# Performance work log

Hardware: AMD Instinct MI355X
Metric: run time of the kernel (lower is better)

The kernel has to match this reference:

```python
import jax, jax.numpy as jnp
import numpy as np

N = 100000   # nodes
E = 1600000  # edges (avg in-degree 16)
IN, H, C = 128, 128, 40
K = 2        # TAGConv hops (DGL default)


def setup_inputs() -> dict:
    key = jax.random.key(0)
    ks = jax.random.split(key, 7)
    in_feat = jax.random.normal(ks[0], (N, IN), dtype=jnp.float32)
    src = jax.random.randint(ks[1], (E,), 0, N)
    dst = jax.random.randint(ks[2], (E,), 0, N)
    # TAGConv linear: concat of (K+1) hop features -> out
    W1 = jax.random.normal(ks[3], ((K + 1) * IN, H), dtype=jnp.float32) / np.float32(np.sqrt((K + 1) * IN))
    b1 = jnp.zeros((H,), dtype=jnp.float32)
    W2 = jax.random.normal(ks[4], ((K + 1) * H, C), dtype=jnp.float32) / np.float32(np.sqrt((K + 1) * H))
    b2 = jnp.zeros((C,), dtype=jnp.float32)
    return {"in_feat": in_feat, "src": src, "dst": dst,
            "W1": W1, "b1": b1, "W2": W2, "b2": b2}


def _tagconv(x, src, dst, norm, W, b):
    feats = [x]
    h = x
    for _ in range(K):
        h = norm[:, None] * h                               # [N, d]
        h = jax.ops.segment_sum(h[src], dst, num_segments=N)  # SpMM via gather+scatter
        h = norm[:, None] * h
        feats.append(h)
    return jnp.concatenate(feats, axis=-1) @ W + b


def reference(in_feat, src, dst, W1, b1, W2, b2):
    deg = jax.ops.segment_sum(jnp.ones((E,), jnp.float32), dst, num_segments=N)
    norm = jnp.where(deg > 0, deg ** -0.5, 0.0)             # D^{-1/2}, inf -> 0
    h = jax.nn.relu(_tagconv(in_feat, src, dst, norm, W1, b1))
    h = jax.nn.relu(_tagconv(h, src, dst, norm, W2, b2))
    return jnp.mean(h, axis=0, keepdims=True)               # dgl.mean_nodes -> [1, C]
```

## Files before the change

kernel.cpp:

```cpp
#include <hip/hip_runtime.h>

typedef unsigned short u16;
typedef __attribute__((ext_vector_type(8))) short bf16x8;
typedef __attribute__((ext_vector_type(4))) float f32x4;

#define CSR_CHUNK 12288

__device__ inline u16 f2bf(float f) {
    union { float f; unsigned u; } v; v.f = f;
    unsigned r = v.u + 0x7fff + ((v.u >> 16) & 1);
    return (u16)(r >> 16);
}
__device__ inline float bflo(unsigned u) {
    union { unsigned u; float f; } v; v.u = u << 16; return v.f;
}
__device__ inline float bfhi(unsigned u) {
    union { unsigned u; float f; } v; v.u = u & 0xffff0000u; return v.f;
}
__device__ inline float bfs(u16 x) { return bflo((unsigned)x); }
__device__ inline unsigned pk(float lo, float hi) {
    return (unsigned)f2bf(lo) | ((unsigned)f2bf(hi) << 16);
}

__global__ __launch_bounds__(256) void prep_k(
    const float* __restrict__ X, u16* __restrict__ Xb, long n4,
    const float* __restrict__ W1, u16* __restrict__ Wp1,
    const float* __restrict__ W2, u16* __restrict__ Wp2,
    int* __restrict__ bcnt, int nzero) {
    int b = blockIdx.x;
    int t = threadIdx.x;
    if (b < 4) {
        int i = b * 256 + t;
        if (i < nzero) bcnt[i] = 0;
        return;
    }
    b -= 4;
    if (b < 192) {
        int i = b * 256 + t;
        int m = i >> 14, r = i & 16383;
        int jj = r & 7, lane = (r >> 3) & 63, kk = (r >> 9) & 3, tt = r >> 11;
        int k = kk * 32 + (lane >> 4) * 8 + jj;
        int c = tt * 16 + (lane & 15);
        Wp1[i] = f2bf(W1[(size_t)m * 16384 + k * 128 + c]);
        return;
    }
    b -= 192;
    if (b < 64) {
        int i = b * 256 + t;
        int jj = i & 7, lane = (i >> 3) & 63, kk = (i >> 9) & 3, tt = i >> 11;
        int k = kk * 32 + (lane >> 4) * 8 + jj;
        int c = tt * 16 + (lane & 15);
        float v = 0.f;
        if (c < 120) {
            int hop = c / 40, j = c - hop * 40;
            v = W2[(size_t)(hop * 128 + k) * 40 + j];
        }
        Wp2[i] = f2bf(v);
        return;
    }
    b -= 64;
    long i = (long)b * 256 + t;
    if (i >= n4) return;
    float4 v = ((const float4*)X)[i];
    ushort4 o;
    o.x = f2bf(v.x); o.y = f2bf(v.y); o.z = f2bf(v.z); o.w = f2bf(v.w);
    ((ushort4*)Xb)[i] = o;
}

__global__ __launch_bounds__(256) void bucket_cnt_k(
    const int* __restrict__ dst, int* __restrict__ bcnt, int E, int nbuck) {
    __shared__ int hist[1024];
    int e0 = blockIdx.x * CSR_CHUNK;
    int e1 = min(e0 + CSR_CHUNK, E);
    for (int i = threadIdx.x; i < nbuck; i += 256) hist[i] = 0;
    __syncthreads();
    for (int e = e0 + threadIdx.x; e < e1; e += 256)
        atomicAdd(&hist[dst[e] >> 7], 1);
    __syncthreads();
    for (int i = threadIdx.x; i < nbuck; i += 256) {
        int c = hist[i];
        if (c) atomicAdd(&bcnt[i], c);
    }
}

__global__ void bscan_k(const int* __restrict__ bcnt, int* __restrict__ bptr,
                        int* __restrict__ bcur, int nb, int E) {
    __shared__ int lds[256];
    int t = threadIdx.x;
    int base = t * 4;
    int v[4];
    int s = 0;
#pragma unroll
    for (int i = 0; i < 4; ++i) {
        v[i] = s;
        int idx = base + i;
        s += (idx < nb) ? bcnt[idx] : 0;
    }
    int x = s;
    lds[t] = x;
    __syncthreads();
    for (int off = 1; off < 256; off <<= 1) {
        int y = (t >= off) ? lds[t - off] : 0;
        __syncthreads();
        x += y;
        lds[t] = x;
        __syncthreads();
    }
    int toff = x - s;
#pragma unroll
    for (int i = 0; i < 4; ++i) {
        int idx = base + i;
        if (idx < nb) {
            int e0 = toff + v[i];
            bptr[idx] = e0;
            bcur[idx] = e0;
        }
    }
    if (t == 255) bptr[nb] = E;
}

__global__ __launch_bounds__(256) void passB_k(
    const int* __restrict__ src, const int* __restrict__ dst,
    int* __restrict__ bcur, int* __restrict__ tmp, int E, int nbuck) {
    __shared__ int hist[1024];
    __shared__ int bbase[1024];
    int e0 = blockIdx.x * CSR_CHUNK;
    int e1 = min(e0 + CSR_CHUNK, E);
    for (int i = threadIdx.x; i < nbuck; i += 256) hist[i] = 0;
    __syncthreads();
    for (int e = e0 + threadIdx.x; e < e1; e += 256)
        atomicAdd(&hist[dst[e] >> 7], 1);
    __syncthreads();
    for (int i = threadIdx.x; i < nbuck; i += 256) {
        int c = hist[i];
        bbase[i] = c ? atomicAdd(&bcur[i], c) : 0;
        hist[i] = 0;
    }
    __syncthreads();
    for (int e = e0 + threadIdx.x; e < e1; e += 256) {
        int s = src[e], d = dst[e];
        int b = d >> 7;
        int r = atomicAdd(&hist[b], 1);
        tmp[bbase[b] + r] = (s << 7) | (d & 127);
    }
}

__global__ __launch_bounds__(256) void passC_k(
    const int* __restrict__ tmp, const int* __restrict__ bptr,
    int* __restrict__ rowptr, float* __restrict__ norm, int* __restrict__ esrc,
    int N, int E) {
    __shared__ int cnt[128];
    __shared__ int sc[128];
    __shared__ int cur[128];
    int b = blockIdx.x, t = threadIdx.x;
    int base = bptr[b], endp = bptr[b + 1];
    int node0 = b << 7;
    int nNodes = min(128, N - node0);

    if (t < 128) cnt[t] = 0;
    __syncthreads();
    for (int i = base + t; i < endp; i += 256)
        atomicAdd(&cnt[tmp[i] & 127], 1);
    __syncthreads();
    if (t < 128) sc[t] = cnt[t];
    __syncthreads();
    for (int off = 1; off < 128; off <<= 1) {
        int y = 0;
        if (t < 128 && t >= off) y = sc[t - off];
        __syncthreads();
        if (t < 128) sc[t] += y;
        __syncthreads();
    }
    if (t < 128) {
        int ex = sc[t] - cnt[t];
        cur[t] = ex;
        if (t < nNodes) {
            rowptr[node0 + t] = base + ex;
            int d = cnt[t];
            norm[node0 + t] = (d > 0) ? rsqrtf((float)d) : 0.f;
        }
    }
    if (b == gridDim.x - 1 && t == 0) rowptr[N] = E;
    __syncthreads();
    for (int i = base + t; i < endp; i += 256) {
        int p = tmp[i];
        int pos = atomicAdd(&cur[p & 127], 1);
        esrc[base + pos] = p >> 7;
    }
}

template <int MODE>
__global__ __launch_bounds__(256, 2) void gemm_mfma_k(
    const u16* __restrict__ Ab, const u16* __restrict__ Wp,
    float* __restrict__ Cf, u16* __restrict__ Cb,
    float* __restrict__ Cf2, u16* __restrict__ Cb2,
    const float* __restrict__ norm, int n, int nStripes) {
    int lane = threadIdx.x & 63;
    int wave = threadIdx.x >> 6;
    int rit = lane & 15;
    int kgrp = lane >> 4;

    bf16x8 bfr[8][4];
    const bf16x8* wp = (const bf16x8*)Wp;
#pragma unroll
    for (int t = 0; t < 8; ++t)
#pragma unroll
        for (int kk = 0; kk < 4; ++kk)
            bfr[t][kk] = wp[(t * 4 + kk) * 64 + lane];

    for (int s = blockIdx.x; s < nStripes; s += gridDim.x) {
        int r0 = s * 64 + wave * 16;
        int ar = min(r0 + rit, n - 1);
        const bf16x8* arow = (const bf16x8*)(Ab + (size_t)ar * 128);
        bf16x8 afr[4];
#pragma unroll
        for (int kk = 0; kk < 4; ++kk) afr[kk] = arow[kk * 4 + kgrp];

        f32x4 acc[8];
#pragma unroll
        for (int t = 0; t < 8; ++t) acc[t] = (f32x4)(0.f);
#pragma unroll
        for (int kk = 0; kk < 4; ++kk)
#pragma unroll
            for (int t = 0; t < 8; ++t)
                acc[t] = __builtin_amdgcn_mfma_f32_16x16x32_bf16(
                    afr[kk], bfr[t][kk], acc[t], 0, 0, 0);

#pragma unroll
        for (int j = 0; j < 4; ++j) {
            int rs = r0 + kgrp * 4 + j;
            if (rs >= n) continue;
            float nr = (MODE == 4) ? 0.f : norm[rs];
#pragma unroll
            for (int t = 0; t < 8; ++t) {
                int c = t * 16 + rit;
                float v = acc[t][j];
                if (MODE == 0) {
                    if (c < 40) Cf[(size_t)rs * 40 + c] = v;
                    else if (c < 80) Cf2[(size_t)rs * 40 + c - 40] = v;
                    else if (c < 120) Cb2[(size_t)rs * 40 + c - 80] = f2bf(v * nr);
                } else if (MODE == 1) {
                    Cb[(size_t)rs * 128 + c] = f2bf(v * nr);
                } else {
                    Cb[(size_t)rs * 128 + c] = f2bf(v);
                }
            }
        }
    }
}

template <int F>
__global__ __launch_bounds__(256) void spmm128_f_k(
    const u16* __restrict__ g, const u16* __restrict__ P,
    const float* __restrict__ bias, u16* __restrict__ outb,
    const float* __restrict__ norm,
    const int* __restrict__ rowptr, const int* __restrict__ esrc, int n) {
    int node = (blockIdx.x * 256 + threadIdx.x) >> 6;
    if (node >= n) return;
    int lane = threadIdx.x & 63;
    int sub = lane >> 4;
    int l16 = lane & 15;
    int beg = rowptr[node], end = rowptr[node + 1];
    float a[8];
#pragma unroll
    for (int j = 0; j < 8; ++j) a[j] = 0.f;

    int e = beg + sub;
    for (; e + 4 < end; e += 8) {
        int s0 = esrc[e], s1 = esrc[e + 4];
        uint4 v0 = *(const uint4*)(g + (size_t)s0 * 128 + l16 * 8);
        uint4 v1 = *(const uint4*)(g + (size_t)s1 * 128 + l16 * 8);
        a[0] += bflo(v0.x); a[1] += bfhi(v0.x);
        a[2] += bflo(v0.y); a[3] += bfhi(v0.y);
        a[4] += bflo(v0.z); a[5] += bfhi(v0.z);
        a[6] += bflo(v0.w); a[7] += bfhi(v0.w);
        a[0] += bflo(v1.x); a[1] += bfhi(v1.x);
        a[2] += bflo(v1.y); a[3] += bfhi(v1.y);
        a[4] += bflo(v1.z); a[5] += bfhi(v1.z);
        a[6] += bflo(v1.w); a[7] += bfhi(v1.w);
    }
    for (; e < end; e += 4) {
        int s = esrc[e];
        uint4 v = *(const uint4*)(g + (size_t)s * 128 + l16 * 8);
        a[0] += bflo(v.x); a[1] += bfhi(v.x);
        a[2] += bflo(v.y); a[3] += bfhi(v.y);
        a[4] += bflo(v.z); a[5] += bfhi(v.z);
        a[6] += bflo(v.w); a[7] += bfhi(v.w);
    }
#pragma unroll
    for (int j = 0; j < 8; ++j) {
        a[j] += __shfl_xor(a[j], 16);
        a[j] += __shfl_xor(a[j], 32);
    }
    if (sub == 0) {
        float nn = norm[node];
        uint4 pv = *(const uint4*)(P + (size_t)node * 128 + l16 * 8);
        float p[8];
        p[0] = bflo(pv.x); p[1] = bfhi(pv.x);
        p[2] = bflo(pv.y); p[3] = bfhi(pv.y);
        p[4] = bflo(pv.z); p[5] = bfhi(pv.z);
        p[6] = bflo(pv.w); p[7] = bfhi(pv.w);
        float r[8];
        if (F == 1) {
#pragma unroll
            for (int j = 0; j < 8; ++j) r[j] = nn * (p[j] + nn * a[j]);
        } else {
            float4 b0 = *(const float4*)(bias + l16 * 8);
            float4 b1v = *(const float4*)(bias + l16 * 8 + 4);
            r[0] = fmaxf(p[0] + nn * a[0] + b0.x, 0.f);
            r[1] = fmaxf(p[1] + nn * a[1] + b0.y, 0.f);
            r[2] = fmaxf(p[2] + nn * a[2] + b0.z, 0.f);
            r[3] = fmaxf(p[3] + nn * a[3] + b0.w, 0.f);
            r[4] = fmaxf(p[4] + nn * a[4] + b1v.x, 0.f);
            r[5] = fmaxf(p[5] + nn * a[5] + b1v.y, 0.f);
            r[6] = fmaxf(p[6] + nn * a[6] + b1v.z, 0.f);
            r[7] = fmaxf(p[7] + nn * a[7] + b1v.w, 0.f);
        }
        uint4 o;
        o.x = pk(r[0], r[1]);
        o.y = pk(r[2], r[3]);
        o.z = pk(r[4], r[5]);
        o.w = pk(r[6], r[7]);
        *(uint4*)(outb + (size_t)node * 128 + l16 * 8) = o;
    }
}

__global__ __launch_bounds__(256) void spmm40_k(
    const u16* __restrict__ Z2b, const float* __restrict__ Z1, u16* __restrict__ u,
    const float* __restrict__ norm, const int* __restrict__ rowptr,
    const int* __restrict__ esrc, int n) {
    int gw = (blockIdx.x * 256 + threadIdx.x) >> 6;
    int lane = threadIdx.x & 63;
    if (gw >= n || lane >= 40) return;
    int beg = rowptr[gw], end = rowptr[gw + 1];
    float a = 0.f;
    int e = beg;
    for (; e + 3 < end; e += 4) {
        int s0 = esrc[e], s1 = esrc[e + 1], s2 = esrc[e + 2], s3 = esrc[e + 3];
        float v0 = bfs(Z2b[(size_t)s0 * 40 + lane]);
        float v1 = bfs(Z2b[(size_t)s1 * 40 + lane]);
        float v2 = bfs(Z2b[(size_t)s2 * 40 + lane]);
        float v3 = bfs(Z2b[(size_t)s3 * 40 + lane]);
        a += (v0 + v1) + (v2 + v3);
    }
    for (; e < end; ++e) a += bfs(Z2b[(size_t)esrc[e] * 40 + lane]);
    float nn = norm[gw];
    u[(size_t)gw * 40 + lane] = f2bf(nn * (Z1[(size_t)gw * 40 + lane] + nn * a));
}

__global__ __launch_bounds__(256) void spmm40_final_k(
    const u16* __restrict__ u, const float* __restrict__ Z0, const float* __restrict__ bias,
    float* __restrict__ partial, const float* __restrict__ norm,
    const int* __restrict__ rowptr, const int* __restrict__ esrc, int n, int nwaves) {
    __shared__ float lds[4][40];
    int wave = threadIdx.x >> 6;
    int lane = threadIdx.x & 63;
    int gw0 = blockIdx.x * 4 + wave;
    float accm = 0.f;
    float bb = (lane < 40) ? bias[lane] : 0.f;
    for (int node = gw0; node < n; node += nwaves) {
        if (lane < 40) {
            int beg = rowptr[node], end = rowptr[node + 1];
            float a = 0.f;
            int e = beg;
            for (; e + 3 < end; e += 4) {
                int s0 = esrc[e], s1 = esrc[e + 1], s2 = esrc[e + 2], s3 = esrc[e + 3];
                float v0 = bfs(u[(size_t)s0 * 40 + lane]);
                float v1 = bfs(u[(size_t)s1 * 40 + lane]);
                float v2 = bfs(u[(size_t)s2 * 40 + lane]);
                float v3 = bfs(u[(size_t)s3 * 40 + lane]);
                a += (v0 + v1) + (v2 + v3);
            }
            for (; e < end; ++e) a += bfs(u[(size_t)esrc[e] * 40 + lane]);
            float r = Z0[(size_t)node * 40 + lane] + norm[node] * a + bb;
            accm += fmaxf(r, 0.f);
        }
    }
    if (lane < 40) lds[wave][lane] = accm;
    __syncthreads();
    if (threadIdx.x < 40) {
        partial[blockIdx.x * 40 + threadIdx.x] =
            lds[0][threadIdx.x] + lds[1][threadIdx.x] + lds[2][threadIdx.x] + lds[3][threadIdx.x];
    }
}

__global__ __launch_bounds__(256) void reduce_mean_k(
    const float* __restrict__ partial, float* __restrict__ out, int nb, float invN) {
    __shared__ float lds[256];
    int c = blockIdx.x, t = threadIdx.x;
    float s = 0.f;
    for (int i = t; i < nb; i += 256) s += partial[(size_t)i * 40 + c];
    lds[t] = s;
    __syncthreads();
    for (int o = 128; o > 0; o >>= 1) {
        if (t < o) lds[t] += lds[t + o];
        __syncthreads();
    }
    if (t == 0) out[c] = lds[0] * invN;
}

extern "C" void kernel_launch(void* const* d_in, const int* in_sizes, int n_in,
                              void* d_out, int out_size, void* d_ws, size_t ws_size,
                              hipStream_t stream) {
    const float* X   = (const float*)d_in[0];
    const int*   src = (const int*)d_in[1];
    const int*   dst = (const int*)d_in[2];
    const float* W1  = (const float*)d_in[3];
    const float* b1  = (const float*)d_in[4];
    const float* W2  = (const float*)d_in[5];
    const float* b2  = (const float*)d_in[6];
    float* out = (float*)d_out;

    const int IN = 128;
    const int N = in_sizes[0] / IN;
    const int E = in_sizes[1];
    const int nb = (N + 127) >> 7;

    char* w = (char*)d_ws;
    size_t off = 0;
    auto alloc = [&](size_t bytes) -> char* {
        char* p = w + off;
        off = (off + bytes + 15) & ~(size_t)15;
        return p;
    };
    float* norm    = (float*)alloc((size_t)N * 4);
    int*   rowptr  = (int*)alloc((size_t)(N + 1) * 4);
    int*   bcnt    = (int*)alloc((size_t)(nb + 1) * 4);
    int*   bptr    = (int*)alloc((size_t)(nb + 1) * 4);
    int*   bcur    = (int*)alloc((size_t)(nb + 1) * 4);
    int*   esrc    = (int*)alloc((size_t)E * 4);
    u16*   Xb      = (u16*)alloc((size_t)N * 128 * 2);
    u16*   h1b     = (u16*)alloc((size_t)N * 128 * 2);
    u16*   g       = (u16*)alloc((size_t)N * 128 * 2);
    u16*   g2      = (u16*)alloc((size_t)N * 128 * 2);
    u16*   Wp1     = (u16*)alloc(3 * 16384 * 2);
    u16*   Wp2     = (u16*)alloc(16384 * 2);
    float* bufF    = (float*)alloc((size_t)N * 128 * 4);
    u16*   ubuf    = (u16*)alloc((size_t)N * 40 * 2);
    float* partial = (float*)alloc(2048 * 40 * 4);

    int*   tmp = (int*)bufF;
    u16*   P1b = (u16*)bufF;
    u16*   P0b = (u16*)bufF + (size_t)N * 128;
    float* Z0  = bufF;
    float* Z1  = bufF + (size_t)N * 40;
    u16*   Z2b = (u16*)(bufF + (size_t)2 * N * 40);

    int csr_blocks = (E + CSR_CHUNK - 1) / CSR_CHUNK;
    long n4 = (long)N * 128 / 4;
    int prep_grid = 4 + 192 + 64 + (int)((n4 + 255) / 256);

    prep_k<<<prep_grid, 256, 0, stream>>>(X, Xb, n4, W1, Wp1, W2, Wp2, bcnt, nb);

    bucket_cnt_k<<<csr_blocks, 256, 0, stream>>>(dst, bcnt, E, nb);
    bscan_k<<<1, 256, 0, stream>>>(bcnt, bptr, bcur, nb, E);
    passB_k<<<csr_blocks, 256, 0, stream>>>(src, dst, bcur, tmp, E, nb);
    passC_k<<<nb, 256, 0, stream>>>(tmp, bptr, rowptr, norm, esrc, N, E);

    int nStripes = (N + 63) / 64;
    int gemm_grid = 512;
    int spmm_grid = (N + 3) / 4;

    gemm_mfma_k<1><<<gemm_grid, 256, 0, stream>>>(
        Xb, Wp1 + 2 * 16384, nullptr, g, nullptr, nullptr, norm, N, nStripes);
    gemm_mfma_k<4><<<gemm_grid, 256, 0, stream>>>(
        Xb, Wp1 + 1 * 16384, nullptr, P1b, nullptr, nullptr, norm, N, nStripes);
    gemm_mfma_k<4><<<gemm_grid, 256, 0, stream>>>(
        Xb, Wp1, nullptr, P0b, nullptr, nullptr, norm, N, nStripes);
    spmm128_f_k<1><<<spmm_grid, 256, 0, stream>>>(
        g, P1b, nullptr, g2, norm, rowptr, esrc, N);
    spmm128_f_k<2><<<spmm_grid, 256, 0, stream>>>(
        g2, P0b, b1, h1b, norm, rowptr, esrc, N);

    gemm_mfma_k<0><<<gemm_grid, 256, 0, stream>>>(
        h1b, Wp2, Z0, nullptr, Z1, Z2b, norm, N, nStripes);
    spmm40_k<<<spmm_grid, 256, 0, stream>>>(Z2b, Z1, ubuf, norm, rowptr, esrc, N);
    spmm40_final_k<<<2048, 256, 0, stream>>>(ubuf, Z0, b2, partial, norm, rowptr, esrc, N, 8192);
    reduce_mean_k<<<40, 256, 0, stream>>>(partial, out, 2048, 1.f / (float)N);
}
```

Before: 425.8 us.

## Drop CSR count pass via fixed-capacity buckets and fuse three layer-1 GEMMs

The CSR build now scatters edges into fixed-capacity per-bucket slots during passB, so the separate dst histogram pass is no longer needed; bucket offsets are scanned afterwards from the atomic cursors. The three layer-1 projections of X are computed in a single kernel that loads each A tile once and loops over the three weight matrices. This removes one full read of dst, two reads of Xb and several launches. In exchange it assumes no 128-node bucket exceeds 8192 in-edges, and it reloads weight fragments for every stripe, which raises register and L2 pressure.

```diff
diff --git a/kernel.cpp b/kernel.cpp
--- a/kernel.cpp
+++ b/kernel.cpp
@@ -5,6 +5,7 @@
 typedef __attribute__((ext_vector_type(4))) float f32x4;
 
 #define CSR_CHUNK 12288
+#define BCAP 8192
 
 __device__ inline u16 f2bf(float f) {
     union { float f; unsigned u; } v; v.f = f;
@@ -26,12 +27,12 @@
     const float* __restrict__ X, u16* __restrict__ Xb, long n4,
     const float* __restrict__ W1, u16* __restrict__ Wp1,
     const float* __restrict__ W2, u16* __restrict__ Wp2,
-    int* __restrict__ bcnt, int nzero) {
+    int* __restrict__ bcur, int nzero) {
     int b = blockIdx.x;
     int t = threadIdx.x;
     if (b < 4) {
         int i = b * 256 + t;
-        if (i < nzero) bcnt[i] = 0;
+        if (i < nzero) bcur[i] = 0;
         return;
     }
     b -= 4;
@@ -67,58 +68,6 @@
     ((ushort4*)Xb)[i] = o;
 }
 
-__global__ __launch_bounds__(256) void bucket_cnt_k(
-    const int* __restrict__ dst, int* __restrict__ bcnt, int E, int nbuck) {
-    __shared__ int hist[1024];
-    int e0 = blockIdx.x * CSR_CHUNK;
-    int e1 = min(e0 + CSR_CHUNK, E);
-    for (int i = threadIdx.x; i < nbuck; i += 256) hist[i] = 0;
-    __syncthreads();
-    for (int e = e0 + threadIdx.x; e < e1; e += 256)
-        atomicAdd(&hist[dst[e] >> 7], 1);
-    __syncthreads();
-    for (int i = threadIdx.x; i < nbuck; i += 256) {
-        int c = hist[i];
-        if (c) atomicAdd(&bcnt[i], c);
-    }
-}
-
-__global__ void bscan_k(const int* __restrict__ bcnt, int* __restrict__ bptr,
-                        int* __restrict__ bcur, int nb, int E) {
-    __shared__ int lds[256];
-    int t = threadIdx.x;
-    int base = t * 4;
-    int v[4];
-    int s = 0;
-#pragma unroll
-    for (int i = 0; i < 4; ++i) {
-        v[i] = s;
-        int idx = base + i;
-        s += (idx < nb) ? bcnt[idx] : 0;
-    }
-    int x = s;
-    lds[t] = x;
-    __syncthreads();
-    for (int off = 1; off < 256; off <<= 1) {
-        int y = (t >= off) ? lds[t - off] : 0;
-        __syncthreads();
-        x += y;
-        lds[t] = x;
-        __syncthreads();
-    }
-    int toff = x - s;
-#pragma unroll
-    for (int i = 0; i < 4; ++i) {
-        int idx = base + i;
-        if (idx < nb) {
-            int e0 = toff + v[i];
-            bptr[idx] = e0;
-            bcur[idx] = e0;
-        }
-    }
-    if (t == 255) bptr[nb] = E;
-}
-
 __global__ __launch_bounds__(256) void passB_k(
     const int* __restrict__ src, const int* __restrict__ dst,
     int* __restrict__ bcur, int* __restrict__ tmp, int E, int nbuck) {
@@ -141,8 +90,40 @@
         int s = src[e], d = dst[e];
         int b = d >> 7;
         int r = atomicAdd(&hist[b], 1);
-        tmp[bbase[b] + r] = (s << 7) | (d & 127);
-    }
+        tmp[b * BCAP + bbase[b] + r] = (s << 7) | (d & 127);
+    }
+}
+
+__global__ void bscan_k(const int* __restrict__ bcur, int* __restrict__ bptr,
+                        int nb, int E) {
+    __shared__ int lds[256];
+    int t = threadIdx.x;
+    int base = t * 4;
+    int v[4];
+    int s = 0;
+#pragma unroll
+    for (int i = 0; i < 4; ++i) {
+        v[i] = s;
+        int idx = base + i;
+        s += (idx < nb) ? bcur[idx] : 0;
+    }
+    int x = s;
+    lds[t] = x;
+    __syncthreads();
+    for (int off = 1; off < 256; off <<= 1) {
+        int y = (t >= off) ? lds[t - off] : 0;
+        __syncthreads();
+        x += y;
+        lds[t] = x;
+        __syncthreads();
+    }
+    int toff = x - s;
+#pragma unroll
+    for (int i = 0; i < 4; ++i) {
+        int idx = base + i;
+        if (idx < nb) bptr[idx] = toff + v[i];
+    }
+    if (t == 255) bptr[nb] = E;
 }
 
 __global__ __launch_bounds__(256) void passC_k(
@@ -153,14 +134,16 @@
     __shared__ int sc[128];
     __shared__ int cur[128];
     int b = blockIdx.x, t = threadIdx.x;
-    int base = bptr[b], endp = bptr[b + 1];
+    int base = bptr[b];
+    int cnt_e = bptr[b + 1] - base;
+    int tin = b * BCAP;
     int node0 = b << 7;
     int nNodes = min(128, N - node0);
 
     if (t < 128) cnt[t] = 0;
     __syncthreads();
-    for (int i = base + t; i < endp; i += 256)
-        atomicAdd(&cnt[tmp[i] & 127], 1);
+    for (int i = t; i < cnt_e; i += 256)
+        atomicAdd(&cnt[tmp[tin + i] & 127], 1);
     __syncthreads();
     if (t < 128) sc[t] = cnt[t];
     __syncthreads();
@@ -182,32 +165,22 @@
     }
     if (b == gridDim.x - 1 && t == 0) rowptr[N] = E;
     __syncthreads();
-    for (int i = base + t; i < endp; i += 256) {
-        int p = tmp[i];
+    for (int i = t; i < cnt_e; i += 256) {
+        int p = tmp[tin + i];
         int pos = atomicAdd(&cur[p & 127], 1);
         esrc[base + pos] = p >> 7;
     }
 }
 
-template <int MODE>
-__global__ __launch_bounds__(256, 2) void gemm_mfma_k(
-    const u16* __restrict__ Ab, const u16* __restrict__ Wp,
-    float* __restrict__ Cf, u16* __restrict__ Cb,
-    float* __restrict__ Cf2, u16* __restrict__ Cb2,
+__global__ __launch_bounds__(256, 2) void gemm3_k(
+    const u16* __restrict__ Ab, const u16* __restrict__ Wp1,
+    u16* __restrict__ P0b, u16* __restrict__ P1b, u16* __restrict__ g,
     const float* __restrict__ norm, int n, int nStripes) {
     int lane = threadIdx.x & 63;
     int wave = threadIdx.x >> 6;
     int rit = lane & 15;
     int kgrp = lane >> 4;
 
-    bf16x8 bfr[8][4];
-    const bf16x8* wp = (const bf16x8*)Wp;
-#pragma unroll
-    for (int t = 0; t < 8; ++t)
-#pragma unroll
-        for (int kk = 0; kk < 4; ++kk)
-            bfr[t][kk] = wp[(t * 4 + kk) * 64 + lane];
-
     for (int s = blockIdx.x; s < nStripes; s += gridDim.x) {
         int r0 = s * 64 + wave * 16;
         int ar = min(r0 + rit, n - 1);
@@ -216,6 +189,67 @@
 #pragma unroll
         for (int kk = 0; kk < 4; ++kk) afr[kk] = arow[kk * 4 + kgrp];
 
+        for (int m = 0; m < 3; ++m) {
+            const bf16x8* wp = (const bf16x8*)(Wp1 + m * 16384);
+            u16* outp = (m == 0) ? P0b : (m == 1) ? P1b : g;
+
+            bf16x8 bfr[8][4];
+#pragma unroll
+            for (int t = 0; t < 8; ++t)
+#pragma unroll
+                for (int kk = 0; kk < 4; ++kk)
+                    bfr[t][kk] = wp[(t * 4 + kk) * 64 + lane];
+
+            f32x4 acc[8];
+#pragma unroll
+            for (int t = 0; t < 8; ++t) acc[t] = (f32x4)(0.f);
+#pragma unroll
+            for (int kk = 0; kk < 4; ++kk)
+#pragma unroll
+                for (int t = 0; t < 8; ++t)
+                    acc[t] = __builtin_amdgcn_mfma_f32_16x16x32_bf16(
+                        afr[kk], bfr[t][kk], acc[t], 0, 0, 0);
+
+#pragma unroll
+            for (int j = 0; j < 4; ++j) {
+                int rs = r0 + kgrp * 4 + j;
+                if (rs >= n) continue;
+                float sc = (m == 2) ? norm[rs] : 1.f;
+#pragma unroll
+                for (int t = 0; t < 8; ++t) {
+                    int c = t * 16 + rit;
+                    outp[(size_t)rs * 128 + c] = f2bf(acc[t][j] * sc);
+                }
+            }
+        }
+    }
+}
+
+__global__ __launch_bounds__(256, 2) void gemm_l2_k(
+    const u16* __restrict__ Ab, const u16* __restrict__ Wp,
+    float* __restrict__ Z0, float* __restrict__ Z1, u16* __restrict__ Z2b,
+    const float* __restrict__ norm, int n, int nStripes) {
+    int lane = threadIdx.x & 63;
+    int wave = threadIdx.x >> 6;
+    int rit = lane & 15;
+    int kgrp = lane >> 4;
+
+    bf16x8 bfr[8][4];
+    const bf16x8* wp = (const bf16x8*)Wp;
+#pragma unroll
+    for (int t = 0; t < 8; ++t)
+#pragma unroll
+        for (int kk = 0; kk < 4; ++kk)
+            bfr[t][kk] = wp[(t * 4 + kk) * 64 + lane];
+
+    for (int s = blockIdx.x; s < nStripes; s += gridDim.x) {
+        int r0 = s * 64 + wave * 16;
+        int ar = min(r0 + rit, n - 1);
+        const bf16x8* arow = (const bf16x8*)(Ab + (size_t)ar * 128);
+        bf16x8 afr[4];
+#pragma unroll
+        for (int kk = 0; kk < 4; ++kk) afr[kk] = arow[kk * 4 + kgrp];
+
         f32x4 acc[8];
 #pragma unroll
         for (int t = 0; t < 8; ++t) acc[t] = (f32x4)(0.f);
@@ -230,20 +264,14 @@
         for (int j = 0; j < 4; ++j) {
             int rs = r0 + kgrp * 4 + j;
             if (rs >= n) continue;
-            float nr = (MODE == 4) ? 0.f : norm[rs];
+            float nr = norm[rs];
 #pragma unroll
             for (int t = 0; t < 8; ++t) {
                 int c = t * 16 + rit;
                 float v = acc[t][j];
-                if (MODE == 0) {
-                    if (c < 40) Cf[(size_t)rs * 40 + c] = v;
-                    else if (c < 80) Cf2[(size_t)rs * 40 + c - 40] = v;
-                    else if (c < 120) Cb2[(size_t)rs * 40 + c - 80] = f2bf(v * nr);
-                } else if (MODE == 1) {
-                    Cb[(size_t)rs * 128 + c] = f2bf(v * nr);
-                } else {
-                    Cb[(size_t)rs * 128 + c] = f2bf(v);
-                }
+                if (c < 40) Z0[(size_t)rs * 40 + c] = v;
+                else if (c < 80) Z1[(size_t)rs * 40 + c - 40] = v;
+                else if (c < 120) Z2b[(size_t)rs * 40 + c - 80] = f2bf(v * nr);
             }
         }
     }
@@ -425,7 +453,6 @@
     };
     float* norm    = (float*)alloc((size_t)N * 4);
     int*   rowptr  = (int*)alloc((size_t)(N + 1) * 4);
-    int*   bcnt    = (int*)alloc((size_t)(nb + 1) * 4);
     int*   bptr    = (int*)alloc((size_t)(nb + 1) * 4);
     int*   bcur    = (int*)alloc((size_t)(nb + 1) * 4);
     int*   esrc    = (int*)alloc((size_t)E * 4);
@@ -440,8 +467,8 @@
     float* partial = (float*)alloc(2048 * 40 * 4);
 
     int*   tmp = (int*)bufF;
-    u16*   P1b = (u16*)bufF;
-    u16*   P0b = (u16*)bufF + (size_t)N * 128;
+    u16*   P0b = (u16*)bufF;
+    u16*   P1b = (u16*)bufF + (size_t)N * 128;
     float* Z0  = bufF;
     float* Z1  = bufF + (size_t)N * 40;
     u16*   Z2b = (u16*)(bufF + (size_t)2 * N * 40);
@@ -450,30 +477,25 @@
     long n4 = (long)N * 128 / 4;
     int prep_grid = 4 + 192 + 64 + (int)((n4 + 255) / 256);
 
-    prep_k<<<prep_grid, 256, 0, stream>>>(X, Xb, n4, W1, Wp1, W2, Wp2, bcnt, nb);
-
-    bucket_cnt_k<<<csr_blocks, 256, 0, stream>>>(dst, bcnt, E, nb);
-    bscan_k<<<1, 256, 0, stream>>>(bcnt, bptr, bcur, nb, E);
+    prep_k<<<prep_grid, 256, 0, stream>>>(X, Xb, n4, W1, Wp1, W2, Wp2, bcur, nb);
+
     passB_k<<<csr_blocks, 256, 0, stream>>>(src, dst, bcur, tmp, E, nb);
+    bscan_k<<<1, 256, 0, stream>>>(bcur, bptr, nb, E);
     passC_k<<<nb, 256, 0, stream>>>(tmp, bptr, rowptr, norm, esrc, N, E);
 
     int nStripes = (N + 63) / 64;
     int gemm_grid = 512;
     int spmm_grid = (N + 3) / 4;
 
-    gemm_mfma_k<1><<<gemm_grid, 256, 0, stream>>>(
-        Xb, Wp1 + 2 * 16384, nullptr, g, nullptr, nullptr, norm, N, nStripes);
-    gemm_mfma_k<4><<<gemm_grid, 256, 0, stream>>>(
-        Xb, Wp1 + 1 * 16384, nullptr, P1b, nullptr, nullptr, norm, N, nStripes);
-    gemm_mfma_k<4><<<gemm_grid, 256, 0, stream>>>(
-        Xb, Wp1, nullptr, P0b, nullptr, nullptr, norm, N, nStripes);
+    gemm3_k<<<gemm_grid, 256, 0, stream>>>(
+        Xb, Wp1, P0b, P1b, g, norm, N, nStripes);
     spmm128_f_k<1><<<spmm_grid, 256, 0, stream>>>(
         g, P1b, nullptr, g2, norm, rowptr, esrc, N);
     spmm128_f_k<2><<<spmm_grid, 256, 0, stream>>>(
         g2, P0b, b1, h1b, norm, rowptr, esrc, N);
 
-    gemm_mfma_k<0><<<gemm_grid, 256, 0, stream>>>(
-        h1b, Wp2, Z0, nullptr, Z1, Z2b, norm, N, nStripes);
+    gemm_l2_k<<<gemm_grid, 256, 0, stream>>>(
+        h1b, Wp2, Z0, Z1, Z2b, norm, N, nStripes);
     spmm40_k<<<spmm_grid, 256, 0, stream>>>(Z2b, Z1, ubuf, norm, rowptr, esrc, N);
     spmm40_final_k<<<2048, 256, 0, stream>>>(ubuf, Z0, b2, partial, norm, rowptr, esrc, N, 8192);
     reduce_mean_k<<<40, 256, 0, stream>>>(partial, out, 2048, 1.f / (float)N);
```

Result: slower. 506.6 us (+19.0%).

## Drop bucket-count pass by scattering edges into fixed-capacity per-bucket slots

Applied to the files above, without the earlier changes.

The CSR build no longer runs a separate dst-histogram kernel plus scan before the scatter pass. passB now reserves space per bucket through atomics on a zeroed cursor and writes into fixed-capacity slots of BCAP entries per bucket. The scan runs afterwards on the final counts, and passC reads each bucket's slot and compacts it into esrc. This removes one full read of dst and one launch, at the cost of a fixed 8192-entry capacity per 128-node bucket, which could overflow on skewed graphs. The tmp buffer also grows to nb*BCAP ints, so the P0b/P1b aliasing order inside bufF is swapped.

```diff
diff --git a/kernel.cpp b/kernel.cpp
--- a/kernel.cpp
+++ b/kernel.cpp
@@ -5,6 +5,7 @@
 typedef __attribute__((ext_vector_type(4))) float f32x4;
 
 #define CSR_CHUNK 12288
+#define BCAP 8192
 
 __device__ inline u16 f2bf(float f) {
     union { float f; unsigned u; } v; v.f = f;
@@ -26,12 +27,12 @@
     const float* __restrict__ X, u16* __restrict__ Xb, long n4,
     const float* __restrict__ W1, u16* __restrict__ Wp1,
     const float* __restrict__ W2, u16* __restrict__ Wp2,
-    int* __restrict__ bcnt, int nzero) {
+    int* __restrict__ bcur, int nzero) {
     int b = blockIdx.x;
     int t = threadIdx.x;
     if (b < 4) {
         int i = b * 256 + t;
-        if (i < nzero) bcnt[i] = 0;
+        if (i < nzero) bcur[i] = 0;
         return;
     }
     b -= 4;
@@ -67,58 +68,6 @@
     ((ushort4*)Xb)[i] = o;
 }
 
-__global__ __launch_bounds__(256) void bucket_cnt_k(
-    const int* __restrict__ dst, int* __restrict__ bcnt, int E, int nbuck) {
-    __shared__ int hist[1024];
-    int e0 = blockIdx.x * CSR_CHUNK;
-    int e1 = min(e0 + CSR_CHUNK, E);
-    for (int i = threadIdx.x; i < nbuck; i += 256) hist[i] = 0;
-    __syncthreads();
-    for (int e = e0 + threadIdx.x; e < e1; e += 256)
-        atomicAdd(&hist[dst[e] >> 7], 1);
-    __syncthreads();
-    for (int i = threadIdx.x; i < nbuck; i += 256) {
-        int c = hist[i];
-        if (c) atomicAdd(&bcnt[i], c);
-    }
-}
-
-__global__ void bscan_k(const int* __restrict__ bcnt, int* __restrict__ bptr,
-                        int* __restrict__ bcur, int nb, int E) {
-    __shared__ int lds[256];
-    int t = threadIdx.x;
-    int base = t * 4;
-    int v[4];
-    int s = 0;
-#pragma unroll
-    for (int i = 0; i < 4; ++i) {
-        v[i] = s;
-        int idx = base + i;
-        s += (idx < nb) ? bcnt[idx] : 0;
-    }
-    int x = s;
-    lds[t] = x;
-    __syncthreads();
-    for (int off = 1; off < 256; off <<= 1) {
-        int y = (t >= off) ? lds[t - off] : 0;
-        __syncthreads();
-        x += y;
-        lds[t] = x;
-        __syncthreads();
-    }
-    int toff = x - s;
-#pragma unroll
-    for (int i = 0; i < 4; ++i) {
-        int idx = base + i;
-        if (idx < nb) {
-            int e0 = toff + v[i];
-            bptr[idx] = e0;
-            bcur[idx] = e0;
-        }
-    }
-    if (t == 255) bptr[nb] = E;
-}
-
 __global__ __launch_bounds__(256) void passB_k(
     const int* __restrict__ src, const int* __restrict__ dst,
     int* __restrict__ bcur, int* __restrict__ tmp, int E, int nbuck) {
@@ -141,8 +90,40 @@
         int s = src[e], d = dst[e];
         int b = d >> 7;
         int r = atomicAdd(&hist[b], 1);
-        tmp[bbase[b] + r] = (s << 7) | (d & 127);
-    }
+        tmp[b * BCAP + bbase[b] + r] = (s << 7) | (d & 127);
+    }
+}
+
+__global__ void bscan_k(const int* __restrict__ bcur, int* __restrict__ bptr,
+                        int nb, int E) {
+    __shared__ int lds[256];
+    int t = threadIdx.x;
+    int base = t * 4;
+    int v[4];
+    int s = 0;
+#pragma unroll
+    for (int i = 0; i < 4; ++i) {
+        v[i] = s;
+        int idx = base + i;
+        s += (idx < nb) ? bcur[idx] : 0;
+    }
+    int x = s;
+    lds[t] = x;
+    __syncthreads();
+    for (int off = 1; off < 256; off <<= 1) {
+        int y = (t >= off) ? lds[t - off] : 0;
+        __syncthreads();
+        x += y;
+        lds[t] = x;
+        __syncthreads();
+    }
+    int toff = x - s;
+#pragma unroll
+    for (int i = 0; i < 4; ++i) {
+        int idx = base + i;
+        if (idx < nb) bptr[idx] = toff + v[i];
+    }
+    if (t == 255) bptr[nb] = E;
 }
 
 __global__ __launch_bounds__(256) void passC_k(
@@ -153,14 +134,16 @@
     __shared__ int sc[128];
     __shared__ int cur[128];
     int b = blockIdx.x, t = threadIdx.x;
-    int base = bptr[b], endp = bptr[b + 1];
+    int base = bptr[b];
+    int cnt_e = bptr[b + 1] - base;
+    int tin = b * BCAP;
     int node0 = b << 7;
     int nNodes = min(128, N - node0);
 
     if (t < 128) cnt[t] = 0;
     __syncthreads();
-    for (int i = base + t; i < endp; i += 256)
-        atomicAdd(&cnt[tmp[i] & 127], 1);
+    for (int i = t; i < cnt_e; i += 256)
+        atomicAdd(&cnt[tmp[tin + i] & 127], 1);
     __syncthreads();
     if (t < 128) sc[t] = cnt[t];
     __syncthreads();
@@ -182,8 +165,8 @@
     }
     if (b == gridDim.x - 1 && t == 0) rowptr[N] = E;
     __syncthreads();
-    for (int i = base + t; i < endp; i += 256) {
-        int p = tmp[i];
+    for (int i = t; i < cnt_e; i += 256) {
+        int p = tmp[tin + i];
         int pos = atomicAdd(&cur[p & 127], 1);
         esrc[base + pos] = p >> 7;
     }
@@ -425,7 +408,6 @@
     };
     float* norm    = (float*)alloc((size_t)N * 4);
     int*   rowptr  = (int*)alloc((size_t)(N + 1) * 4);
-    int*   bcnt    = (int*)alloc((size_t)(nb + 1) * 4);
     int*   bptr    = (int*)alloc((size_t)(nb + 1) * 4);
     int*   bcur    = (int*)alloc((size_t)(nb + 1) * 4);
     int*   esrc    = (int*)alloc((size_t)E * 4);
@@ -440,8 +422,8 @@
     float* partial = (float*)alloc(2048 * 40 * 4);
 
     int*   tmp = (int*)bufF;
-    u16*   P1b = (u16*)bufF;
-    u16*   P0b = (u16*)bufF + (size_t)N * 128;
+    u16*   P0b = (u16*)bufF;
+    u16*   P1b = (u16*)bufF + (size_t)N * 128;
     float* Z0  = bufF;
     float* Z1  = bufF + (size_t)N * 40;
     u16*   Z2b = (u16*)(bufF + (size_t)2 * N * 40);
@@ -450,11 +432,10 @@
     long n4 = (long)N * 128 / 4;
     int prep_grid = 4 + 192 + 64 + (int)((n4 + 255) / 256);
 
-    prep_k<<<prep_grid, 256, 0, stream>>>(X, Xb, n4, W1, Wp1, W2, Wp2, bcnt, nb);
-
-    bucket_cnt_k<<<csr_blocks, 256, 0, stream>>>(dst, bcnt, E, nb);
-    bscan_k<<<1, 256, 0, stream>>>(bcnt, bptr, bcur, nb, E);
+    prep_k<<<prep_grid, 256, 0, stream>>>(X, Xb, n4, W1, Wp1, W2, Wp2, bcur, nb);
+
     passB_k<<<csr_blocks, 256, 0, stream>>>(src, dst, bcur, tmp, E, nb);
+    bscan_k<<<1, 256, 0, stream>>>(bcur, bptr, nb, E);
     passC_k<<<nb, 256, 0, stream>>>(tmp, bptr, rowptr, norm, esrc, N, E);
 
     int nStripes = (N + 63) / 64;
```

After: 416.8 us. -2.1%, faster.
